# Kernel tuning notes

Measured on AMD Instinct MI355X. Metric: run time of the kernel, lower is better.

Reference implementation:

```python
import jax, jax.numpy as jnp
import numpy as np

N, F_IN, PRE, K = 400000, 64, 32, 6
EDGE = [32, 32]


def _dense_params(key, fan_in, fan_out):
    kw, kb = jax.random.split(key)
    W = jax.random.normal(kw, (fan_in, fan_out), jnp.float32) / np.sqrt(fan_in).astype(np.float32)
    b = jnp.zeros((fan_out,), jnp.float32)
    return W, b


def setup_inputs() -> dict:
    key = jax.random.key(0)
    ks = jax.random.split(key, 10)
    x = jax.random.normal(ks[0], (N, F_IN), jnp.float32)
    distsq = jax.random.uniform(ks[1], (N, K), jnp.float32)
    nidx = jax.random.randint(ks[2], (N, K), 0, N, jnp.int64)
    Wp, bp = _dense_params(ks[3], F_IN, PRE)
    # edge MLP: input K*(PRE+1) -> 32 -> 32 -> K
    We1, be1 = _dense_params(ks[4], K * (PRE + 1), EDGE[0])
    We2, be2 = _dense_params(ks[5], EDGE[0], EDGE[1])
    We3, be3 = _dense_params(ks[6], EDGE[1], K)
    # self MLP: F_IN -> 32 -> 32 -> 1
    Ws1, bs1 = _dense_params(ks[7], F_IN, EDGE[0])
    Ws2, bs2 = _dense_params(ks[8], EDGE[0], EDGE[1])
    Ws3, bs3 = _dense_params(ks[9], EDGE[1], 1)
    return dict(x=x, distsq=distsq, nidx=nidx, Wp=Wp, bp=bp,
                We1=We1, be1=be1, We2=We2, be2=be2, We3=We3, be3=be3,
                Ws1=Ws1, bs1=bs1, Ws2=Ws2, bs2=bs2, Ws3=Ws3, bs3=bs3)


def _forward(x, distsq, nidx, Wp, bp, We1, be1, We2, be2, We3, be3,
             Ws1, bs1, Ws2, bs2, Ws3, bs3):
    # pre-dense: [N, PRE]
    x_p = jax.nn.elu(x @ Wp + bp)
    # gather neighbors; select(nidx, x_n, 0.0) masks nidx<0 to 0.0
    safe_idx = jnp.maximum(nidx, 0)
    gathered = x_p[safe_idx]                              # [N, K, PRE]
    gathered = jnp.where(nidx[:, :, None] < 0, 0.0, gathered)
    diff = x_p[:, None, :] - gathered                     # [N, K, PRE]
    xn = jnp.concatenate([diff, distsq[:, :, None]], axis=2)  # [N, K, PRE+1]
    xn = xn.reshape(xn.shape[0], K * (PRE + 1))
    xn = jax.nn.elu(xn @ We1 + be1)
    xn = jax.nn.elu(xn @ We2 + be2)
    xn = xn @ We3 + be3                                   # [N, K]
    xs = jax.nn.elu(x @ Ws1 + bs1)
    xs = jax.nn.elu(xs @ Ws2 + bs2)
    xs = xs @ Ws3 + bs3                                   # [N, 1]
    out = jnp.concatenate([xs, xn], axis=1)               # [N, K+1]
    return jax.nn.softmax(out, axis=1)


def reference(x, distsq, nidx, Wp, bp, We1, be1, We2, be2, We3, be3,
              Ws1, bs1, Ws2, bs2, Ws3, bs3):
    return _forward(x, distsq, nidx, Wp, bp, We1, be1, We2, be2, We3, be3,
                    Ws1, bs1, Ws2, bs2, Ws3, bs3)
```

## Files before the change

kernel.cpp:

```cpp
#include <hip/hip_runtime.h>
#include <hip/hip_bf16.h>
#include <math.h>

typedef __hip_bfloat16 bf16;
typedef __attribute__((ext_vector_type(8))) __bf16 bf16x8;
typedef __attribute__((ext_vector_type(4))) float f32x4;
typedef unsigned int u32x4 __attribute__((ext_vector_type(4)));

#define F_IN 64
#define KNB 6

#define WOFF_BP   2048
#define WOFF_BE2  9472
#define WOFF_BE3  9696
#define WOFF_BS1  11776
#define WOFF_BS2  12832
#define WOFF_BS3  12896
#define FLAGS_OFF 13056
#define FRAG_OFF  14592
#define NFRAG_PRE 11
#define NFRAG_EDGE 19
#define STAGE_OFF 24576

#define MFMA(a, b, c) __builtin_amdgcn_mfma_f32_16x16x32_bf16(a, b, c, 0, 0, 0)

__device__ __forceinline__ float b2f(bf16 v) { return __bfloat162float(v); }
__device__ __forceinline__ float eluf(float v) { return v > 0.f ? v : __expf(v) - 1.f; }

__device__ __forceinline__ ushort f2bu(float v) {
  __bf16 b = (__bf16)v; ushort u; __builtin_memcpy(&u, &b, 2); return u;
}

union U8 { uint4 u; bf16x8 v; ushort s[8]; };

__device__ __forceinline__ uint4 ntload16(const void* p) {
  u32x4 t = __builtin_nontemporal_load((const u32x4*)p);
  uint4 r; r.x = t.x; r.y = t.y; r.z = t.z; r.w = t.w; return r;
}

__device__ __forceinline__ bf16x8 ldfrag(const ushort* fr, int f) {
  U8 u; u.u = *(const uint4*)(fr + f * 512 + (threadIdx.x & 63) * 8);
  return u.v;
}

__device__ __forceinline__ int permo(int m, int t) { return 8 * (m >> 2) + (m & 3) + 4 * t; }

__global__ void setupK(const ushort* xb, const int* ni,
                       const void* Wp, const void* bp, const void* We1, const void* be1,
                       const void* We2, const void* be2, const void* We3, const void* be3,
                       const void* Ws1, const void* bs1, const void* Ws2, const void* bs2,
                       const void* Ws3, const void* bs3, float* w) {
  __shared__ int sbf;
  int t = threadIdx.x;
  if (t < 64) {
    int bad = 0;
    for (int i = t; i < 256; i += 64) {
      float v = __uint_as_float(((unsigned)xb[i]) << 16);
      if (!(fabsf(v) < 100.f)) bad++;
    }
    unsigned long long bm = __ballot(bad > 0);
    if (t == 0) sbf = (__popcll(bm) < 4) ? 1 : 0;
  }
  __syncthreads();
  int bf = sbf;
  auto rv = [&](const void* p, long i) -> float {
    return bf ? b2f(((const bf16*)p)[i]) : ((const float*)p)[i];
  };
  if (blockIdx.x == 0) {
    if (t < 64) {
      unsigned long long hm = __ballot(ni[2 * t + 1] != 0);
      if (t == 0) {
        ((int*)(w + FLAGS_OFF))[0] = bf;
        ((int*)(w + FLAGS_OFF))[1] = (hm == 0ULL) ? 1 : 0;
      }
    }
    const void* bsrc[6] = {bp, bs1, bs2, bs3, be2, be3};
    const int bn[6] = {32, 32, 32, 1, 32, 6};
    const int bo[6] = {WOFF_BP, WOFF_BS1, WOFF_BS2, WOFF_BS3, WOFF_BE2, WOFF_BE3};
    for (int a = 0; a < 6; a++)
      for (int i = t; i < bn[a]; i += blockDim.x)
        w[bo[a] + i] = rv(bsrc[a], i);
  }
  ushort* fbv = (ushort*)(w + FRAG_OFF);
  int total = (NFRAG_PRE + NFRAG_EDGE) * 512;
  for (int i = blockIdx.x * blockDim.x + t; i < total; i += gridDim.x * blockDim.x) {
    int f = i >> 9, e = i & 511;
    int lane = e >> 3, j = e & 7;
    int mm = lane & 15, qq = lane >> 4;
    int k = qq * 8 + j;
    float v = 0.f;
    if (f < 4) { int s = f >> 1, tt = f & 1; v = rv(Wp, (long)(32 * s + k) * 32 + permo(mm, tt)); }
    else if (f < 8) { int s = (f - 4) >> 1, tt = f & 1; v = rv(Ws1, (long)(32 * s + k) * 32 + permo(mm, tt)); }
    else if (f < 10) { int tt = f & 1; v = rv(Ws2, (long)k * 32 + permo(mm, tt)); }
    else if (f == 10) { v = (mm == 0) ? rv(Ws3, k) : 0.f; }
    else if (f < 23) { int kn = (f - 11) >> 1, tt = (f - 11) & 1;
                       v = -rv(We1, (long)(kn * 33 + k) * 32 + permo(mm, tt)); }
    else if (f < 25) { int tt = f - 23; float s = 0.f;
#pragma unroll
                       for (int kn = 0; kn < KNB; kn++)
                         s += rv(We1, (long)(kn * 33 + k) * 32 + permo(mm, tt));
                       v = s; }
    else if (f < 27) { int tt = f - 25; int o = permo(mm, tt);
                       v = (k < 6) ? rv(We1, (long)(k * 33 + 32) * 32 + o)
                                   : (k == 6 ? rv(be1, o) : 0.f); }
    else if (f < 29) { int tt = f - 27; v = rv(We2, (long)k * 32 + permo(mm, tt)); }
    else { v = (mm < KNB) ? rv(We3, (long)k * 6 + mm) : 0.f; }
    fbv[i] = f2bu(v);
  }
}

template <bool BF16>
__device__ void pre_tiles(const void* xv, const float* __restrict__ w,
                          ushort* __restrict__ xp, float* __restrict__ xs,
                          int n_nodes, const ushort* __restrict__ fr) {
  int lane = threadIdx.x & 63;
  int m = lane & 15, q = lane >> 4;
  float bp8[8], bs18[8], bs28[8];
#pragma unroll
  for (int j = 0; j < 8; j++) {
    bp8[j]  = w[WOFF_BP  + 8 * q + j];
    bs18[j] = w[WOFF_BS1 + 8 * q + j];
    bs28[j] = w[WOFF_BS2 + 8 * q + j];
  }
  float bs3 = w[WOFF_BS3];
  long T = ((long)n_nodes + 15) >> 4;
  long wid = (long)((blockIdx.x * blockDim.x + threadIdx.x) >> 6);
  long nw = (long)((gridDim.x * blockDim.x) >> 6);
  f32x4 zero = {0.f, 0.f, 0.f, 0.f};

  uint4 bufA[4], bufB[4];
  auto loadraw = [&](uint4* r, long tt) {
    long row = tt * 16 + m; if (row >= n_nodes) row = n_nodes - 1;
    if (BF16) {
      const ushort* p = (const ushort*)xv + row * F_IN + q * 8;
      r[0] = ntload16(p);
      r[1] = ntload16(p + 32);
    } else {
      const float* p = (const float*)xv + row * F_IN + q * 8;
      r[0] = ntload16(p);      r[1] = ntload16(p + 4);
      r[2] = ntload16(p + 32); r[3] = ntload16(p + 36);
    }
  };
  auto mkfrag = [&](const uint4* r, int s) -> bf16x8 {
    if (BF16) { U8 u; u.u = r[s]; return u.v; }
    float f0[8];
    __builtin_memcpy(f0, r + 2 * s, 32);
    bf16x8 out;
#pragma unroll
    for (int j = 0; j < 8; j++) out[j] = (__bf16)f0[j];
    return out;
  };
  auto body = [&](uint4* cur, uint4* nxt, long t) {
    long tn = t + nw;
    if (tn < T) loadraw(nxt, tn);
    long n0 = t * 16;
    long row = n0 + m; if (row >= n_nodes) row = n_nodes - 1;
    bf16x8 x0 = mkfrag(cur, 0), x1 = mkfrag(cur, 1);
    f32x4 aP[2], aS[2];
#pragma unroll
    for (int tt = 0; tt < 2; tt++) {
      aP[tt] = MFMA(ldfrag(fr, 0 + tt), x0, zero);
      aP[tt] = MFMA(ldfrag(fr, 2 + tt), x1, aP[tt]);
      aS[tt] = MFMA(ldfrag(fr, 4 + tt), x0, zero);
      aS[tt] = MFMA(ldfrag(fr, 6 + tt), x1, aS[tt]);
    }
    U8 o1;
#pragma unroll
    for (int j = 0; j < 8; j++) o1.s[j] = f2bu(eluf(aP[j >> 2][j & 3] + bp8[j]));
    *(uint4*)(xp + row * 32 + q * 8) = o1.u;
    bf16x8 s1e;
#pragma unroll
    for (int j = 0; j < 8; j++) s1e[j] = (__bf16)eluf(aS[j >> 2][j & 3] + bs18[j]);
    f32x4 a2[2];
#pragma unroll
    for (int tt = 0; tt < 2; tt++) a2[tt] = MFMA(ldfrag(fr, 8 + tt), s1e, zero);
    bf16x8 s2e;
#pragma unroll
    for (int j = 0; j < 8; j++) s2e[j] = (__bf16)eluf(a2[j >> 2][j & 3] + bs28[j]);
    f32x4 a3 = MFMA(ldfrag(fr, 10), s2e, zero);
    if (q == 0) {
      long orow = n0 + m;
      if (orow < n_nodes) xs[orow] = a3[0] + bs3;
    }
  };
  long t = wid;
  if (t < T) loadraw(bufA, t);
  while (t < T) {
    body(bufA, bufB, t);
    t += nw; if (t >= T) break;
    body(bufB, bufA, t);
    t += nw;
  }
}

__launch_bounds__(256)
__global__ void preK(const void* xv, const float* __restrict__ w,
                     const int* __restrict__ flags,
                     ushort* __restrict__ xp, float* __restrict__ xs, int n_nodes) {
  __shared__ uint4 fsh[NFRAG_PRE * 64];
  const uint4* fbv = (const uint4*)((const ushort*)(w + FRAG_OFF));
  for (int i = threadIdx.x; i < NFRAG_PRE * 64; i += blockDim.x) fsh[i] = fbv[i];
  __syncthreads();
  const ushort* fr = (const ushort*)fsh;
  if (flags[0]) pre_tiles<true>(xv, w, xp, xs, n_nodes, fr);
  else          pre_tiles<false>(xv, w, xp, xs, n_nodes, fr);
}

struct ETile { U8 nb[KNB]; U8 own; U8 ad; float xsv; };

template <bool BF16>
__device__ void edge_tiles(const ushort* __restrict__ xp, const float* __restrict__ xs,
                           const void* dsv, const int* __restrict__ ni, int i64,
                           const float* __restrict__ w, void* outv, int n_nodes,
                           const ushort* __restrict__ fr) {
  int lane = threadIdx.x & 63;
  int m = lane & 15, q = lane >> 4;
  float b2[8], b3[4];
#pragma unroll
  for (int j = 0; j < 8; j++) b2[j] = w[WOFF_BE2 + 8 * q + j];
#pragma unroll
  for (int r = 0; r < 4; r++) { int o = 4 * q + r; b3[r] = (o < 6) ? w[WOFF_BE3 + o] : 0.f; }

  long T = ((long)n_nodes + 15) >> 4;
  long wid = (long)((blockIdx.x * blockDim.x + threadIdx.x) >> 6);
  long nw = (long)((gridDim.x * blockDim.x) >> 6);
  f32x4 zero = {0.f, 0.f, 0.f, 0.f};
  ETile A, B;
  int Ia[KNB], Ib[KNB];

  auto pidx = [&](int* ix, long tt) {
    long row = tt * 16 + m; if (row >= n_nodes) row = n_nodes - 1;
#pragma unroll
    for (int k = 0; k < KNB; k++)
      ix[k] = i64 ? ni[(row * KNB + k) * 2] : ni[row * KNB + k];
  };
  auto phead = [&](ETile& d, long tt) {
    long row = tt * 16 + m; if (row >= n_nodes) row = n_nodes - 1;
    d.own.u = *(const uint4*)(xp + row * 32 + q * 8);
    d.ad.u.x = 0; d.ad.u.y = 0; d.ad.u.z = 0; d.ad.u.w = 0;
    if (q == 0) {
      if (BF16) {
        const unsigned* dp = (const unsigned*)dsv;
        d.ad.u.x = dp[row * 3 + 0]; d.ad.u.y = dp[row * 3 + 1]; d.ad.u.z = dp[row * 3 + 2];
      } else {
        const float* dp = (const float*)dsv + row * KNB;
#pragma unroll
        for (int k = 0; k < KNB; k++) d.ad.s[k] = f2bu(dp[k]);
      }
      d.ad.s[6] = 0x3F80u;
    }
    d.xsv = xs[row];
  };
  auto pgather = [&](ETile& d, const int* ix) {
#pragma unroll
    for (int k = 0; k < KNB; k++) {
      int v = ix[k];
      long ai = (v < 0 || v >= n_nodes) ? 0 : (long)v;
      uint4 g = *(const uint4*)(xp + ai * 32 + q * 8);
      if (v < 0) { g.x = 0; g.y = 0; g.z = 0; g.w = 0; }
      d.nb[k].u = g;
    }
  };
  auto iterb = [&](ETile& cur, ETile& nxt, int* Iin, int* Iout, long t) {
    long t2 = t + 2 * nw;
    bool h2 = t2 < T;
    if (h2) pidx(Iout, t2);
    f32x4 acc[2];
#pragma unroll
    for (int tt = 0; tt < 2; tt++) {
      acc[tt] = MFMA(ldfrag(fr, 12 + tt), cur.own.v, zero);
      acc[tt] = MFMA(ldfrag(fr, 14 + tt), cur.ad.v, acc[tt]);
#pragma unroll
      for (int k = 0; k < KNB; k++)
        acc[tt] = MFMA(ldfrag(fr, k * 2 + tt), cur.nb[k].v, acc[tt]);
    }
    if (t + nw < T) pgather(nxt, Iin);
    bf16x8 a1;
#pragma unroll
    for (int j = 0; j < 8; j++) a1[j] = (__bf16)eluf(acc[j >> 2][j & 3]);
    f32x4 acc2[2];
#pragma unroll
    for (int tt = 0; tt < 2; tt++) acc2[tt] = MFMA(ldfrag(fr, 16 + tt), a1, zero);
    bf16x8 a2;
#pragma unroll
    for (int j = 0; j < 8; j++) a2[j] = (__bf16)eluf(acc2[j >> 2][j & 3] + b2[j]);
    f32x4 a3 = MFMA(ldfrag(fr, 18), a2, zero);
    float l0 = a3[0] + b3[0], l1 = a3[1] + b3[1], l2 = a3[2] + b3[2], l3 = a3[3] + b3[3];
    float o4 = __shfl(l0, m + 16, 64);
    float o5 = __shfl(l1, m + 16, 64);
    if (lane < 16) {
      long nodeid = t * 16 + lane;
      if (nodeid < n_nodes) {
        float lg[7] = {cur.xsv, l0, l1, l2, l3, o4, o5};
        float mx = lg[0];
#pragma unroll
        for (int i = 1; i < 7; i++) mx = fmaxf(mx, lg[i]);
        float e[7], ssum = 0.f;
#pragma unroll
        for (int i = 0; i < 7; i++) { e[i] = __expf(lg[i] - mx); ssum += e[i]; }
        float inv = 1.f / ssum;
        if (BF16) {
          ushort* o = (ushort*)outv + nodeid * 7;
#pragma unroll
          for (int i = 0; i < 7; i++) o[i] = f2bu(e[i] * inv);
        } else {
          float* o = (float*)outv + nodeid * 7;
#pragma unroll
          for (int i = 0; i < 7; i++) o[i] = e[i] * inv;
        }
      }
    }
    if (h2) phead(cur, t2);
  };
  long t = wid;
  if (t < T) {
    pidx(Ia, t); phead(A, t); pgather(A, Ia);
    if (t + nw < T) { pidx(Ia, t + nw); phead(B, t + nw); }
  }
  while (t < T) {
    iterb(A, B, Ia, Ib, t);
    t += nw; if (t >= T) break;
    iterb(B, A, Ib, Ia, t);
    t += nw;
  }
}

__launch_bounds__(256)
__global__ void edgeK(const ushort* __restrict__ xp, const float* __restrict__ xs,
                      const void* dsv, const int* __restrict__ ni,
                      const float* __restrict__ w, const int* __restrict__ flags,
                      void* outv, int n_nodes) {
  __shared__ uint4 fsh[NFRAG_EDGE * 64];
  const uint4* fbv = (const uint4*)((const ushort*)(w + FRAG_OFF) + NFRAG_PRE * 512);
  for (int i = threadIdx.x; i < NFRAG_EDGE * 64; i += blockDim.x) fsh[i] = fbv[i];
  __syncthreads();
  const ushort* fr = (const ushort*)fsh;
  if (flags[0]) edge_tiles<true>(xp, xs, dsv, ni, flags[1], w, outv, n_nodes, fr);
  else          edge_tiles<false>(xp, xs, dsv, ni, flags[1], w, outv, n_nodes, fr);
}

template <bool BF16>
__device__ __forceinline__ float wval(const void* W, long i) {
  if (BF16) return b2f(((const bf16*)W)[i]);
  return ((const float*)W)[i];
}

__device__ __forceinline__ void block_flags(const ushort* xb, const int* ni, int* sflags) {
  if (threadIdx.x < 64) {
    int t = threadIdx.x;
    int bad = 0;
    for (int i = t; i < 256; i += 64) {
      float v = __uint_as_float(((unsigned)xb[i]) << 16);
      if (!(fabsf(v) < 100.f)) bad++;
    }
    unsigned long long bm = __ballot(bad > 0);
    unsigned long long hm = __ballot(ni[2 * t + 1] != 0);
    if (t == 0) {
      sflags[0] = (__popcll(bm) < 4) ? 1 : 0;
      sflags[1] = (hm == 0ULL) ? 1 : 0;
    }
  }
  __syncthreads();
}

template <bool BF16>
__device__ void node_body(int n, int n_nodes, const void* xv, const void* dsv,
                          const int* __restrict__ ni, int i64,
                          const void* Wp, const void* bp, const void* We1, const void* be1,
                          const void* We2, const void* be2, const void* We3, const void* be3,
                          const void* Ws1, const void* bs1, const void* Ws2, const void* bs2,
                          const void* Ws3, const void* bs3, void* outv) {
  float h[32], s1[32];
#pragma unroll
  for (int o = 0; o < 32; o++) { h[o] = wval<BF16>(bp, o); s1[o] = wval<BF16>(bs1, o); }
  for (int j = 0; j < F_IN; j++) {
    float xj = wval<BF16>(xv, (long)n * F_IN + j);
#pragma unroll
    for (int o = 0; o < 32; o++) {
      h[o]  += xj * wval<BF16>(Wp,  (long)j * 32 + o);
      s1[o] += xj * wval<BF16>(Ws1, (long)j * 32 + o);
    }
  }
  float own[32];
#pragma unroll
  for (int o = 0; o < 32; o++) own[o] = eluf(h[o]);
  float s2[32];
#pragma unroll
  for (int o = 0; o < 32; o++) s2[o] = wval<BF16>(bs2, o);
  for (int j = 0; j < 32; j++) {
    float v = eluf(s1[j]);
#pragma unroll
    for (int o = 0; o < 32; o++) s2[o] += v * wval<BF16>(Ws2, (long)j * 32 + o);
  }
  float xsv = wval<BF16>(bs3, 0);
#pragma unroll
  for (int j = 0; j < 32; j++) xsv += eluf(s2[j]) * wval<BF16>(Ws3, j);

  float h1[32];
#pragma unroll
  for (int o = 0; o < 32; o++) h1[o] = wval<BF16>(be1, o);
  for (int k = 0; k < KNB; k++) {
    long pos = (long)n * KNB + k;
    int idx = i64 ? ni[2 * pos] : ni[pos];
    float mmask = idx < 0 ? 0.f : 1.f;
    long ai = idx < 0 ? 0 : idx;
    if (ai >= n_nodes) ai = 0;
    float nh[32];
#pragma unroll
    for (int o = 0; o < 32; o++) nh[o] = wval<BF16>(bp, o);
    for (int j = 0; j < F_IN; j++) {
      float xj = wval<BF16>(xv, ai * F_IN + j);
#pragma unroll
      for (int o = 0; o < 32; o++) nh[o] += xj * wval<BF16>(Wp, (long)j * 32 + o);
    }
#pragma unroll
    for (int j = 0; j < 32; j++) {
      float d = own[j] - mmask * eluf(nh[j]);
#pragma unroll
      for (int o = 0; o < 32; o++) h1[o] += d * wval<BF16>(We1, ((long)(k * 33 + j)) * 32 + o);
    }
    float dsq = BF16 ? b2f(((const bf16*)dsv)[pos]) : ((const float*)dsv)[pos];
#pragma unroll
    for (int o = 0; o < 32; o++) h1[o] += dsq * wval<BF16>(We1, ((long)(k * 33 + 32)) * 32 + o);
  }
  float h2[32];
#pragma unroll
  for (int o = 0; o < 32; o++) h2[o] = wval<BF16>(be2, o);
  for (int j = 0; j < 32; j++) {
    float v = eluf(h1[j]);
#pragma unroll
    for (int o = 0; o < 32; o++) h2[o] += v * wval<BF16>(We2, (long)j * 32 + o);
  }
  float lg[7];
  lg[0] = xsv;
#pragma unroll
  for (int o = 0; o < 6; o++) lg[1 + o] = wval<BF16>(be3, o);
  for (int j = 0; j < 32; j++) {
    float v = eluf(h2[j]);
#pragma unroll
    for (int o = 0; o < 6; o++) lg[1 + o] += v * wval<BF16>(We3, (long)j * 6 + o);
  }
  float mx = lg[0];
#pragma unroll
  for (int i = 1; i < 7; i++) mx = fmaxf(mx, lg[i]);
  float e[7], ssum = 0.f;
#pragma unroll
  for (int i = 0; i < 7; i++) { e[i] = __expf(lg[i] - mx); ssum += e[i]; }
  float inv = 1.f / ssum;
  if (BF16) {
    bf16* o = (bf16*)outv;
#pragma unroll
    for (int i = 0; i < 7; i++) o[(long)n * 7 + i] = __float2bfloat16(e[i] * inv);
  } else {
    float* o = (float*)outv;
#pragma unroll
    for (int i = 0; i < 7; i++) o[(long)n * 7 + i] = e[i] * inv;
  }
}

__launch_bounds__(256)
__global__ void fused(const void* xv, const void* dsv, const int* __restrict__ ni,
                      const void* Wp, const void* bp, const void* We1, const void* be1,
                      const void* We2, const void* be2, const void* We3, const void* be3,
                      const void* Ws1, const void* bs1, const void* Ws2, const void* bs2,
                      const void* Ws3, const void* bs3, void* outv, int n_nodes) {
  __shared__ int sflags[2];
  block_flags((const ushort*)xv, ni, sflags);
  int n = blockIdx.x * blockDim.x + threadIdx.x;
  if (n >= n_nodes) return;
  if (sflags[0]) node_body<true>(n, n_nodes, xv, dsv, ni, sflags[1], Wp, bp, We1, be1,
                                 We2, be2, We3, be3, Ws1, bs1, Ws2, bs2, Ws3, bs3, outv);
  else           node_body<false>(n, n_nodes, xv, dsv, ni, sflags[1], Wp, bp, We1, be1,
                                  We2, be2, We3, be3, Ws1, bs1, Ws2, bs2, Ws3, bs3, outv);
}

extern "C" void kernel_launch(void* const* d_in, const int* in_sizes, int n_in,
                              void* d_out, int out_size, void* d_ws, size_t ws_size,
                              hipStream_t stream) {
  const void* x      = d_in[0];
  const void* distsq = d_in[1];
  const int*  nidx   = (const int*)d_in[2];

  float* w = (float*)d_ws;
  int* flags = (int*)(w + FLAGS_OFF);
  int n_nodes = in_sizes[0] / F_IN;

  size_t need = (size_t)STAGE_OFF * 4 + (size_t)n_nodes * 64 + (size_t)n_nodes * 4 + 256;
  if (ws_size >= need) {
    setupK<<<32, 256, 0, stream>>>((const ushort*)x, nidx,
                                   d_in[3], d_in[4], d_in[5], d_in[6], d_in[7], d_in[8],
                                   d_in[9], d_in[10], d_in[11], d_in[12], d_in[13], d_in[14],
                                   d_in[15], d_in[16], w);
    ushort* xp = (ushort*)(w + STAGE_OFF);
    float* xs = (float*)(xp + (size_t)n_nodes * 32);
    preK<<<2048, 256, 0, stream>>>(x, w, flags, xp, xs, n_nodes);
    edgeK<<<2048, 256, 0, stream>>>(xp, xs, distsq, nidx, w, flags, d_out, n_nodes);
  } else {
    int grid = (n_nodes + 255) / 256;
    fused<<<grid, 256, 0, stream>>>(x, distsq, nidx, d_in[3], d_in[4], d_in[5], d_in[6],
                                    d_in[7], d_in[8], d_in[9], d_in[10], d_in[11], d_in[12],
                                    d_in[13], d_in[14], d_in[15], d_in[16], d_out, n_nodes);
  }
}
```

Baseline: 252.6 us.

## Deepen pre-kernel prefetch to two tiles ahead and simplify edge-kernel pipeline

```diff
diff --git a/kernel.cpp b/kernel.cpp
--- a/kernel.cpp
+++ b/kernel.cpp
@@ -128,7 +128,7 @@
   long nw = (long)((gridDim.x * blockDim.x) >> 6);
   f32x4 zero = {0.f, 0.f, 0.f, 0.f};
 
-  uint4 bufA[4], bufB[4];
+  uint4 bufA[4], bufB[4], bufC[4];
   auto loadraw = [&](uint4* r, long tt) {
     long row = tt * 16 + m; if (row >= n_nodes) row = n_nodes - 1;
     if (BF16) {
@@ -150,13 +150,14 @@
     for (int j = 0; j < 8; j++) out[j] = (__bf16)f0[j];
     return out;
   };
-  auto body = [&](uint4* cur, uint4* nxt, long t) {
-    long tn = t + nw;
-    if (tn < T) loadraw(nxt, tn);
+  auto body = [&](uint4* cur, uint4* pref, long t) {
+    long tp = t + 2 * nw;
+    if (tp < T) loadraw(pref, tp);
     long n0 = t * 16;
     long row = n0 + m; if (row >= n_nodes) row = n_nodes - 1;
     bf16x8 x0 = mkfrag(cur, 0), x1 = mkfrag(cur, 1);
     f32x4 aP[2], aS[2];
+    __builtin_amdgcn_s_setprio(1);
 #pragma unroll
     for (int tt = 0; tt < 2; tt++) {
       aP[tt] = MFMA(ldfrag(fr, 0 + tt), x0, zero);
@@ -164,6 +165,7 @@
       aS[tt] = MFMA(ldfrag(fr, 4 + tt), x0, zero);
       aS[tt] = MFMA(ldfrag(fr, 6 + tt), x1, aS[tt]);
     }
+    __builtin_amdgcn_s_setprio(0);
     U8 o1;
 #pragma unroll
     for (int j = 0; j < 8; j++) o1.s[j] = f2bu(eluf(aP[j >> 2][j & 3] + bp8[j]));
@@ -185,10 +187,13 @@
   };
   long t = wid;
   if (t < T) loadraw(bufA, t);
+  if (t + nw < T) loadraw(bufB, t + nw);
   while (t < T) {
-    body(bufA, bufB, t);
+    body(bufA, bufC, t);
     t += nw; if (t >= T) break;
     body(bufB, bufA, t);
+    t += nw; if (t >= T) break;
+    body(bufC, bufB, t);
     t += nw;
   }
 }
@@ -226,16 +231,12 @@
   long nw = (long)((gridDim.x * blockDim.x) >> 6);
   f32x4 zero = {0.f, 0.f, 0.f, 0.f};
   ETile A, B;
-  int Ia[KNB], Ib[KNB];
-
-  auto pidx = [&](int* ix, long tt) {
+
+  auto phead = [&](ETile& d, int* idxn, long tt) {
     long row = tt * 16 + m; if (row >= n_nodes) row = n_nodes - 1;
 #pragma unroll
     for (int k = 0; k < KNB; k++)
-      ix[k] = i64 ? ni[(row * KNB + k) * 2] : ni[row * KNB + k];
-  };
-  auto phead = [&](ETile& d, long tt) {
-    long row = tt * 16 + m; if (row >= n_nodes) row = n_nodes - 1;
+      idxn[k] = i64 ? ni[(row * KNB + k) * 2] : ni[row * KNB + k];
     d.own.u = *(const uint4*)(xp + row * 32 + q * 8);
     d.ad.u.x = 0; d.ad.u.y = 0; d.ad.u.z = 0; d.ad.u.w = 0;
     if (q == 0) {
@@ -261,10 +262,11 @@
       d.nb[k].u = g;
     }
   };
-  auto iterb = [&](ETile& cur, ETile& nxt, int* Iin, int* Iout, long t) {
-    long t2 = t + 2 * nw;
-    bool h2 = t2 < T;
-    if (h2) pidx(Iout, t2);
+  auto body = [&](ETile& cur, ETile& nxt, long t) {
+    long tn = t + nw;
+    int idxn[KNB];
+    bool pv = tn < T;
+    if (pv) phead(nxt, idxn, tn);
     f32x4 acc[2];
 #pragma unroll
     for (int tt = 0; tt < 2; tt++) {
@@ -274,7 +276,7 @@
       for (int k = 0; k < KNB; k++)
         acc[tt] = MFMA(ldfrag(fr, k * 2 + tt), cur.nb[k].v, acc[tt]);
     }
-    if (t + nw < T) pgather(nxt, Iin);
+    if (pv) pgather(nxt, idxn);
     bf16x8 a1;
 #pragma unroll
     for (int j = 0; j < 8; j++) a1[j] = (__bf16)eluf(acc[j >> 2][j & 3]);
@@ -310,17 +312,13 @@
         }
       }
     }
-    if (h2) phead(cur, t2);
   };
   long t = wid;
-  if (t < T) {
-    pidx(Ia, t); phead(A, t); pgather(A, Ia);
-    if (t + nw < T) { pidx(Ia, t + nw); phead(B, t + nw); }
-  }
+  if (t < T) { int i0[KNB]; phead(A, i0, t); pgather(A, i0); }
   while (t < T) {
-    iterb(A, B, Ia, Ib, t);
+    body(A, B, t);
     t += nw; if (t >= T) break;
-    iterb(B, A, Ib, Ia, t);
+    body(B, A, t);
     t += nw;
   }
 }
@@ -493,7 +491,7 @@
                                    d_in[15], d_in[16], w);
     ushort* xp = (ushort*)(w + STAGE_OFF);
     float* xs = (float*)(xp + (size_t)n_nodes * 32);
-    preK<<<2048, 256, 0, stream>>>(x, w, flags, xp, xs, n_nodes);
+    preK<<<1024, 256, 0, stream>>>(x, w, flags, xp, xs, n_nodes);
     edgeK<<<2048, 256, 0, stream>>>(xp, xs, distsq, nidx, w, flags, d_out, n_nodes);
   } else {
     int grid = (n_nodes + 255) / 256;
```

Result: no change. 249.7 us (-1.1%).

## Single-buffer edge tile registers and raise wave priority around pre MFMAs

Applied to the files above, without the earlier changes.

```diff
diff --git a/kernel.cpp b/kernel.cpp
--- a/kernel.cpp
+++ b/kernel.cpp
@@ -157,6 +157,7 @@
     long row = n0 + m; if (row >= n_nodes) row = n_nodes - 1;
     bf16x8 x0 = mkfrag(cur, 0), x1 = mkfrag(cur, 1);
     f32x4 aP[2], aS[2];
+    __builtin_amdgcn_s_setprio(1);
 #pragma unroll
     for (int tt = 0; tt < 2; tt++) {
       aP[tt] = MFMA(ldfrag(fr, 0 + tt), x0, zero);
@@ -164,6 +165,7 @@
       aS[tt] = MFMA(ldfrag(fr, 4 + tt), x0, zero);
       aS[tt] = MFMA(ldfrag(fr, 6 + tt), x1, aS[tt]);
     }
+    __builtin_amdgcn_s_setprio(0);
     U8 o1;
 #pragma unroll
     for (int j = 0; j < 8; j++) o1.s[j] = f2bu(eluf(aP[j >> 2][j & 3] + bp8[j]));
@@ -206,8 +208,6 @@
   else          pre_tiles<false>(xv, w, xp, xs, n_nodes, fr);
 }
 
-struct ETile { U8 nb[KNB]; U8 own; U8 ad; float xsv; };
-
 template <bool BF16>
 __device__ void edge_tiles(const ushort* __restrict__ xp, const float* __restrict__ xs,
                            const void* dsv, const int* __restrict__ ni, int i64,
@@ -215,66 +215,70 @@
                            const ushort* __restrict__ fr) {
   int lane = threadIdx.x & 63;
   int m = lane & 15, q = lane >> 4;
-  float b2[8], b3[4];
-#pragma unroll
-  for (int j = 0; j < 8; j++) b2[j] = w[WOFF_BE2 + 8 * q + j];
-#pragma unroll
-  for (int r = 0; r < 4; r++) { int o = 4 * q + r; b3[r] = (o < 6) ? w[WOFF_BE3 + o] : 0.f; }
+  float b2v[8], b3v[4];
+#pragma unroll
+  for (int j = 0; j < 8; j++) b2v[j] = w[WOFF_BE2 + 8 * q + j];
+#pragma unroll
+  for (int r = 0; r < 4; r++) { int o = 4 * q + r; b3v[r] = (o < 6) ? w[WOFF_BE3 + o] : 0.f; }
 
   long T = ((long)n_nodes + 15) >> 4;
   long wid = (long)((blockIdx.x * blockDim.x + threadIdx.x) >> 6);
   long nw = (long)((gridDim.x * blockDim.x) >> 6);
   f32x4 zero = {0.f, 0.f, 0.f, 0.f};
-  ETile A, B;
-  int Ia[KNB], Ib[KNB];
-
-  auto pidx = [&](int* ix, long tt) {
+
+  U8 nb[KNB], own, ad;
+  int idxC[KNB];
+  float xsvA = 0.f, xsvB = 0.f;
+
+  auto pidx = [&](long tt) {
     long row = tt * 16 + m; if (row >= n_nodes) row = n_nodes - 1;
 #pragma unroll
     for (int k = 0; k < KNB; k++)
-      ix[k] = i64 ? ni[(row * KNB + k) * 2] : ni[row * KNB + k];
-  };
-  auto phead = [&](ETile& d, long tt) {
+      idxC[k] = i64 ? ni[(row * KNB + k) * 2] : ni[row * KNB + k];
+  };
+  auto phead = [&](float& xsv, long tt) {
     long row = tt * 16 + m; if (row >= n_nodes) row = n_nodes - 1;
-    d.own.u = *(const uint4*)(xp + row * 32 + q * 8);
-    d.ad.u.x = 0; d.ad.u.y = 0; d.ad.u.z = 0; d.ad.u.w = 0;
+    own.u = *(const uint4*)(xp + row * 32 + q * 8);
+    ad.u.x = 0; ad.u.y = 0; ad.u.z = 0; ad.u.w = 0;
     if (q == 0) {
       if (BF16) {
         const unsigned* dp = (const unsigned*)dsv;
-        d.ad.u.x = dp[row * 3 + 0]; d.ad.u.y = dp[row * 3 + 1]; d.ad.u.z = dp[row * 3 + 2];
+        ad.u.x = dp[row * 3 + 0]; ad.u.y = dp[row * 3 + 1]; ad.u.z = dp[row * 3 + 2];
       } else {
         const float* dp = (const float*)dsv + row * KNB;
 #pragma unroll
-        for (int k = 0; k < KNB; k++) d.ad.s[k] = f2bu(dp[k]);
+        for (int k = 0; k < KNB; k++) ad.s[k] = f2bu(dp[k]);
       }
-      d.ad.s[6] = 0x3F80u;
-    }
-    d.xsv = xs[row];
-  };
-  auto pgather = [&](ETile& d, const int* ix) {
+      ad.s[6] = 0x3F80u;
+    }
+    xsv = xs[row];
+  };
+  auto pgather = [&]() {
 #pragma unroll
     for (int k = 0; k < KNB; k++) {
-      int v = ix[k];
+      int v = idxC[k];
       long ai = (v < 0 || v >= n_nodes) ? 0 : (long)v;
       uint4 g = *(const uint4*)(xp + ai * 32 + q * 8);
       if (v < 0) { g.x = 0; g.y = 0; g.z = 0; g.w = 0; }
-      d.nb[k].u = g;
-    }
-  };
-  auto iterb = [&](ETile& cur, ETile& nxt, int* Iin, int* Iout, long t) {
-    long t2 = t + 2 * nw;
-    bool h2 = t2 < T;
-    if (h2) pidx(Iout, t2);
+      nb[k].u = g;
+    }
+  };
+  auto body = [&](float& xsvCur, float& xsvNxt, long t) {
     f32x4 acc[2];
 #pragma unroll
     for (int tt = 0; tt < 2; tt++) {
-      acc[tt] = MFMA(ldfrag(fr, 12 + tt), cur.own.v, zero);
-      acc[tt] = MFMA(ldfrag(fr, 14 + tt), cur.ad.v, acc[tt]);
+      acc[tt] = MFMA(ldfrag(fr, 12 + tt), own.v, zero);
+      acc[tt] = MFMA(ldfrag(fr, 14 + tt), ad.v, acc[tt]);
 #pragma unroll
       for (int k = 0; k < KNB; k++)
-        acc[tt] = MFMA(ldfrag(fr, k * 2 + tt), cur.nb[k].v, acc[tt]);
-    }
-    if (t + nw < T) pgather(nxt, Iin);
+        acc[tt] = MFMA(ldfrag(fr, k * 2 + tt), nb[k].v, acc[tt]);
+    }
+    long tn = t + nw;
+    if (tn < T) {
+      pgather();
+      phead(xsvNxt, tn);
+      if (tn + nw < T) pidx(tn + nw);
+    }
     bf16x8 a1;
 #pragma unroll
     for (int j = 0; j < 8; j++) a1[j] = (__bf16)eluf(acc[j >> 2][j & 3]);
@@ -283,15 +287,15 @@
     for (int tt = 0; tt < 2; tt++) acc2[tt] = MFMA(ldfrag(fr, 16 + tt), a1, zero);
     bf16x8 a2;
 #pragma unroll
-    for (int j = 0; j < 8; j++) a2[j] = (__bf16)eluf(acc2[j >> 2][j & 3] + b2[j]);
+    for (int j = 0; j < 8; j++) a2[j] = (__bf16)eluf(acc2[j >> 2][j & 3] + b2v[j]);
     f32x4 a3 = MFMA(ldfrag(fr, 18), a2, zero);
-    float l0 = a3[0] + b3[0], l1 = a3[1] + b3[1], l2 = a3[2] + b3[2], l3 = a3[3] + b3[3];
+    float l0 = a3[0] + b3v[0], l1 = a3[1] + b3v[1], l2 = a3[2] + b3v[2], l3 = a3[3] + b3v[3];
     float o4 = __shfl(l0, m + 16, 64);
     float o5 = __shfl(l1, m + 16, 64);
     if (lane < 16) {
       long nodeid = t * 16 + lane;
       if (nodeid < n_nodes) {
-        float lg[7] = {cur.xsv, l0, l1, l2, l3, o4, o5};
+        float lg[7] = {xsvCur, l0, l1, l2, l3, o4, o5};
         float mx = lg[0];
 #pragma unroll
         for (int i = 1; i < 7; i++) mx = fmaxf(mx, lg[i]);
@@ -310,17 +314,16 @@
         }
       }
     }
-    if (h2) phead(cur, t2);
   };
   long t = wid;
   if (t < T) {
-    pidx(Ia, t); phead(A, t); pgather(A, Ia);
-    if (t + nw < T) { pidx(Ia, t + nw); phead(B, t + nw); }
+    pidx(t); pgather(); phead(xsvA, t);
+    if (t + nw < T) pidx(t + nw);
   }
   while (t < T) {
-    iterb(A, B, Ia, Ib, t);
+    body(xsvA, xsvB, t);
     t += nw; if (t >= T) break;
-    iterb(B, A, Ib, Ia, t);
+    body(xsvB, xsvA, t);
     t += nw;
   }
 }
```

After: 254.1 us. About the same (+0.6%).
